# Kernel optimization log

Hardware: AMD Instinct MI355X
Metric: run time of the kernel (lower is better)

## Reference

```python
import jax, jax.numpy as jnp
import numpy as np

EPS = 1e-5

def _ln(x, g, b):
    mu = x.mean(-1, keepdims=True)
    var = ((x - mu) ** 2).mean(-1, keepdims=True)
    return (x - mu) / jnp.sqrt(var + EPS) * g + b


def setup_inputs() -> dict:
    key = jax.random.key(0)
    B, Hd, Wd = 4, 32, 32
    C, heads = 1024, 16
    N = Hd * Wd
    pd = (C // 4) // 4  # DynamicPosBias pos_dim = 64
    hid = 4 * C
    ks = jax.random.split(key, 24)

    def w(k, shape):
        return jax.random.normal(k, shape, jnp.float32) * 0.02

    inp = {
        'x': jax.random.normal(ks[0], (B, N, C), jnp.float32),
        'norm1_g': jnp.ones((C,), jnp.float32), 'norm1_b': jnp.zeros((C,), jnp.float32),
        'q_w': w(ks[1], (C, C)),              # no bias (qkv_bias=False)
        'kv_w': w(ks[2], (C, 2 * C)),
        'proj_w': w(ks[3], (C, C)), 'proj_b': jnp.zeros((C,), jnp.float32),
        'pos_proj_w': w(ks[4], (2, pd)), 'pos_proj_b': jnp.zeros((pd,), jnp.float32),
        'ln1_g': jnp.ones((pd,), jnp.float32), 'ln1_b': jnp.zeros((pd,), jnp.float32),
        'lin1_w': w(ks[5], (pd, pd)), 'lin1_b': jnp.zeros((pd,), jnp.float32),
        'ln2_g': jnp.ones((pd,), jnp.float32), 'ln2_b': jnp.zeros((pd,), jnp.float32),
        'lin2_w': w(ks[6], (pd, pd)), 'lin2_b': jnp.zeros((pd,), jnp.float32),
        'ln3_g': jnp.ones((pd,), jnp.float32), 'ln3_b': jnp.zeros((pd,), jnp.float32),
        'lin3_w': w(ks[7], (pd, heads)), 'lin3_b': jnp.zeros((heads,), jnp.float32),
        'norm2_g': jnp.ones((C,), jnp.float32), 'norm2_b': jnp.zeros((C,), jnp.float32),
        'fc1_w': w(ks[8], (C, hid)), 'fc1_b': jnp.zeros((hid,), jnp.float32),
        'fc2_w': w(ks[9], (hid, C)), 'fc2_b': jnp.zeros((C,), jnp.float32),
        'H': Hd, 'W': Wd,
    }
    return inp


def _rel_pos(H, W):
    # coordinate offsets fed to the bias MLP: [(2H-1)(2W-1), 2]
    ph = np.arange(1 - H, H)
    pw = np.arange(1 - W, W)
    bh, bw = np.meshgrid(ph, pw, indexing='ij')
    biases = np.stack([bh.ravel(), bw.ravel()], axis=1).astype(np.float32)
    # relative position index: [HW, HW]
    ch, cw = np.meshgrid(np.arange(H), np.arange(W), indexing='ij')
    flat = np.stack([ch.ravel(), cw.ravel()])                 # [2, HW]
    rel = flat[:, :, None] - flat[:, None, :]                 # [2, HW, HW]
    rel = rel.transpose(1, 2, 0)
    rel[:, :, 0] += H - 1
    rel[:, :, 1] += W - 1
    rel[:, :, 0] *= 2 * W - 1
    idx = rel.sum(-1)                                         # [HW, HW]
    return jnp.asarray(biases), jnp.asarray(idx)


def reference(x, norm1_g, norm1_b, q_w, kv_w, proj_w, proj_b,
              pos_proj_w, pos_proj_b, ln1_g, ln1_b, lin1_w, lin1_b,
              ln2_g, ln2_b, lin2_w, lin2_b, ln3_g, ln3_b, lin3_w, lin3_b,
              norm2_g, norm2_b, fc1_w, fc1_b, fc2_w, fc2_b, H, W):
    B, N, C = x.shape
    heads = lin3_w.shape[1]
    d = C // heads
    scale = d ** (-0.5)

    # --- HLGAttention (stage_index==4: group_size=(H,W), h0_token=None) ---
    xn = _ln(x, norm1_g, norm1_b)
    q = (xn @ q_w).reshape(B, N, heads, d).transpose(0, 2, 1, 3)   # [B,h,N,d]
    kv = (xn @ kv_w).reshape(B, N, 2, heads, d)
    k = kv[:, :, 0].transpose(0, 2, 1, 3)                          # [B,h,N,d]
    v = kv[:, :, 1].transpose(0, 2, 1, 3)
    attn = jnp.einsum('bhnd,bhmd->bhnm', q, k) * scale

    # dynamic relative position bias via small MLP + gather
    biases, rel_idx = _rel_pos(H, W)
    pos = biases @ pos_proj_w + pos_proj_b
    pos = jax.nn.relu(_ln(pos, ln1_g, ln1_b)) @ lin1_w + lin1_b
    pos = jax.nn.relu(_ln(pos, ln2_g, ln2_b)) @ lin2_w + lin2_b
    pos = jax.nn.relu(_ln(pos, ln3_g, ln3_b)) @ lin3_w + lin3_b    # [(2H-1)(2W-1), heads]
    rpb = pos[rel_idx]                                              # [N,N,heads]
    attn = attn + rpb.transpose(2, 0, 1)[None]

    attn = jax.nn.softmax(attn, axis=-1)
    out = jnp.einsum('bhnm,bhmd->bhnd', attn, v)
    out = out.transpose(0, 2, 1, 3).reshape(B, N, C)
    out = out @ proj_w + proj_b
    x = x + out

    # --- MLP block ---
    h = _ln(x, norm2_g, norm2_b) @ fc1_w + fc1_b
    h = jax.nn.gelu(h, approximate=False)
    x = x + (h @ fc2_w + fc2_b)
    return x
```

## Files before the change

### kernel.cpp

```cpp
#include <hip/hip_runtime.h>
#include <cstdint>
#include <cstddef>

typedef __attribute__((ext_vector_type(8))) __bf16 bf16x8;
typedef __attribute__((ext_vector_type(8))) unsigned short us8;
typedef __attribute__((ext_vector_type(4))) unsigned short us4;
typedef __attribute__((ext_vector_type(4))) float f32x4;
typedef __attribute__((ext_vector_type(16))) float f32x16;

#define DEVI static __device__ __forceinline__

DEVI unsigned short f2bf(float f) {
  union { float f; unsigned u; } v; v.f = f;
  unsigned r = v.u + 0x7fffu + ((v.u >> 16) & 1u);
  return (unsigned short)(r >> 16);
}

DEVI f32x4 mfma16(us8 a, us8 b, f32x4 c) {
  return __builtin_amdgcn_mfma_f32_16x16x32_bf16(
      __builtin_bit_cast(bf16x8, a), __builtin_bit_cast(bf16x8, b), c, 0, 0, 0);
}

DEVI f32x16 mfma32(us8 a, us8 b, f32x16 c) {
  return __builtin_amdgcn_mfma_f32_32x32x16_bf16(
      __builtin_bit_cast(bf16x8, a), __builtin_bit_cast(bf16x8, b), c, 0, 0, 0);
}

DEVI f32x4 fzero4() { f32x4 v = {0.f, 0.f, 0.f, 0.f}; return v; }

DEVI float gelu_f(float v) {
  float z = 0.7978845608f * v * (1.f + 0.044715f * v * v);
  float e = __expf(2.f * z);
  float r = 1.f / (e + 1.f);
  return v * (1.f - r);
}

DEVI unsigned pkbf(float lo, float hi) {
  unsigned r;
  asm("v_cvt_pk_bf16_f32 %0, %1, %2" : "=v"(r) : "v"(lo), "v"(hi));
  return r;
}

DEVI void pswap(unsigned& x, unsigned& y) {
  asm volatile("v_permlane32_swap_b32 %0, %1" : "+v"(x), "+v"(y));
}

DEVI void gload16(const unsigned short* g, unsigned short* l) {
  __builtin_amdgcn_global_load_lds(
      (const __attribute__((address_space(1))) unsigned int*)g,
      (__attribute__((address_space(3))) unsigned int*)l, 16, 0, 0);
}

DEVI void transpose_body(const float* __restrict__ w,
                         unsigned short* __restrict__ wt, int K, int N,
                         int kbi, int nbi, unsigned short (*tile)[65]) {
  const int t = threadIdx.x;
  const int kb = kbi * 64, nb = nbi * 64;
#pragma unroll
  for (int i = 0; i < 4; ++i) {
    int r = i * 16 + (t >> 4);
    int c = (t & 15) * 4;
    float4 v = *(const float4*)(w + (size_t)(kb + r) * N + nb + c);
    tile[r][c + 0] = f2bf(v.x);
    tile[r][c + 1] = f2bf(v.y);
    tile[r][c + 2] = f2bf(v.z);
    tile[r][c + 3] = f2bf(v.w);
  }
  __syncthreads();
#pragma unroll
  for (int i = 0; i < 4; ++i) {
    int n = i * 16 + (t >> 4);
    int k = (t & 15) * 4;
    us4 o;
    o[0] = tile[k + 0][n];
    o[1] = tile[k + 1][n];
    o[2] = tile[k + 2][n];
    o[3] = tile[k + 3][n];
    *(us4*)(wt + (size_t)(nb + n) * K + kb + k) = o;
  }
}

DEVI float pos_layer(float p, const float* __restrict__ g,
                     const float* __restrict__ be, const float* __restrict__ w,
                     const float* __restrict__ bb, int lane) {
  float s = p, sq = p * p;
#pragma unroll
  for (int m = 1; m < 64; m <<= 1) {
    s += __shfl_xor(s, m, 64);
    sq += __shfl_xor(sq, m, 64);
  }
  float mu = s * (1.f / 64.f);
  float var = sq * (1.f / 64.f) - mu * mu;
  float rstd = rsqrtf(var + 1e-5f);
  float y = fmaxf((p - mu) * rstd * g[lane] + be[lane], 0.f);
  float o = bb[lane];
  for (int k = 0; k < 64; ++k) {
    float yk = __shfl(y, k, 64);
    o += yk * w[k * 64 + lane];
  }
  return o;
}

__global__ __launch_bounds__(256)
void prep_kernel(const float* __restrict__ x, const float* __restrict__ n1g,
                 const float* __restrict__ n1b, unsigned short* __restrict__ xn,
                 const float* __restrict__ q_w, const float* __restrict__ kv_w,
                 const float* __restrict__ proj_w,
                 const float* __restrict__ fc1_w,
                 const float* __restrict__ fc2_w,
                 unsigned short* __restrict__ qkvT,
                 unsigned short* __restrict__ projT,
                 unsigned short* __restrict__ fc1T,
                 unsigned short* __restrict__ fc2T,
                 const float* __restrict__ pp_w, const float* __restrict__ pp_b,
                 const float* __restrict__ g1, const float* __restrict__ b1,
                 const float* __restrict__ w1, const float* __restrict__ bb1,
                 const float* __restrict__ g2, const float* __restrict__ b2,
                 const float* __restrict__ w2, const float* __restrict__ bb2,
                 const float* __restrict__ g3, const float* __restrict__ b3,
                 const float* __restrict__ w3, const float* __restrict__ bb3,
                 float* __restrict__ posT) {
  __shared__ unsigned short tile[64][65];
  __shared__ float ss[4], ssq[4];
  const int blk = blockIdx.x;
  const int tid = threadIdx.x;

  if (blk < 4096) {
    const int row = blk;
    const float* xr = x + (size_t)row * 1024;
    float4 v = *(const float4*)(xr + tid * 4);
    float s = v.x + v.y + v.z + v.w;
    float sq = v.x * v.x + v.y * v.y + v.z * v.z + v.w * v.w;
#pragma unroll
    for (int m = 1; m < 64; m <<= 1) {
      s += __shfl_xor(s, m, 64);
      sq += __shfl_xor(sq, m, 64);
    }
    const int wid = tid >> 6, lane = tid & 63;
    if (lane == 0) { ss[wid] = s; ssq[wid] = sq; }
    __syncthreads();
    s = ss[0] + ss[1] + ss[2] + ss[3];
    sq = ssq[0] + ssq[1] + ssq[2] + ssq[3];
    const float mu = s * (1.f / 1024.f);
    const float var = sq * (1.f / 1024.f) - mu * mu;
    const float rstd = rsqrtf(var + 1e-5f);
    const int c = tid * 4;
    float4 gv = *(const float4*)(n1g + c);
    float4 bv = *(const float4*)(n1b + c);
    us4 ov;
    ov[0] = f2bf((v.x - mu) * rstd * gv.x + bv.x);
    ov[1] = f2bf((v.y - mu) * rstd * gv.y + bv.y);
    ov[2] = f2bf((v.z - mu) * rstd * gv.z + bv.z);
    ov[3] = f2bf((v.w - mu) * rstd * gv.w + bv.w);
    *(us4*)(xn + (size_t)row * 1024 + c) = ov;
  } else if (blk < 5089) {
    const int wid = tid >> 6, lane = tid & 63;
    const int row = (blk - 4096) * 4 + wid;
    if (row >= 3969) return;
    const float bh = (float)(row / 63) - 31.f;
    const float bw = (float)(row % 63) - 31.f;
    float p = bh * pp_w[lane] + bw * pp_w[64 + lane] + pp_b[lane];
    p = pos_layer(p, g1, b1, w1, bb1, lane);
    p = pos_layer(p, g2, b2, w2, bb2, lane);
    float s = p, sq = p * p;
#pragma unroll
    for (int m = 1; m < 64; m <<= 1) {
      s += __shfl_xor(s, m, 64);
      sq += __shfl_xor(sq, m, 64);
    }
    float mu = s * (1.f / 64.f);
    float var = sq * (1.f / 64.f) - mu * mu;
    float rstd = rsqrtf(var + 1e-5f);
    float y = fmaxf((p - mu) * rstd * g3[lane] + b3[lane], 0.f);
    float o = 0.f;
    for (int k = 0; k < 64; ++k) {
      float yk = __shfl(y, k, 64);
      o += yk * w3[k * 16 + (lane & 15)];
    }
    if (lane < 16) posT[(size_t)lane * 3969 + row] = o + bb3[lane];
  } else if (blk < 5345) {
    const int lin = blk - 5089;
    transpose_body(q_w, qkvT, 1024, 1024, lin & 15, lin >> 4, tile);
  } else if (blk < 5857) {
    const int lin = blk - 5345;
    transpose_body(kv_w, qkvT + (size_t)1024 * 1024, 1024, 2048, lin & 15,
                   lin >> 4, tile);
  } else if (blk < 6113) {
    const int lin = blk - 5857;
    transpose_body(proj_w, projT, 1024, 1024, lin & 15, lin >> 4, tile);
  } else if (blk < 7137) {
    const int lin = blk - 6113;
    transpose_body(fc1_w, fc1T, 1024, 4096, lin & 15, lin >> 4, tile);
  } else {
    const int lin = blk - 7137;
    transpose_body(fc2_w, fc2T, 4096, 1024, lin & 63, lin >> 6, tile);
  }
}

__global__ __launch_bounds__(256)
void ln_kernel(const float* __restrict__ x, const float* __restrict__ g,
               const float* __restrict__ b, unsigned short* __restrict__ o) {
  const int row = blockIdx.x;
  const int tid = threadIdx.x;
  const float* xr = x + (size_t)row * 1024;
  float4 v = *(const float4*)(xr + tid * 4);
  float s = v.x + v.y + v.z + v.w;
  float sq = v.x * v.x + v.y * v.y + v.z * v.z + v.w * v.w;
#pragma unroll
  for (int m = 1; m < 64; m <<= 1) {
    s += __shfl_xor(s, m, 64);
    sq += __shfl_xor(sq, m, 64);
  }
  __shared__ float ss[4], ssq[4];
  const int wid = tid >> 6, lane = tid & 63;
  if (lane == 0) { ss[wid] = s; ssq[wid] = sq; }
  __syncthreads();
  s = ss[0] + ss[1] + ss[2] + ss[3];
  sq = ssq[0] + ssq[1] + ssq[2] + ssq[3];
  const float mu = s * (1.f / 1024.f);
  const float var = sq * (1.f / 1024.f) - mu * mu;
  const float rstd = rsqrtf(var + 1e-5f);
  const int c = tid * 4;
  float4 gv = *(const float4*)(g + c);
  float4 bv = *(const float4*)(b + c);
  us4 ov;
  ov[0] = f2bf((v.x - mu) * rstd * gv.x + bv.x);
  ov[1] = f2bf((v.y - mu) * rstd * gv.y + bv.y);
  ov[2] = f2bf((v.z - mu) * rstd * gv.z + bv.z);
  ov[3] = f2bf((v.w - mu) * rstd * gv.w + bv.w);
  *(us4*)(o + (size_t)row * 1024 + c) = ov;
}

template <int BM, int BN, bool HAS_BIAS, bool GELU_, bool HAS_RES,
          bool OUT_BF16, bool OUT_F32>
__global__ __launch_bounds__(256)
void gemm_bt(const unsigned short* __restrict__ A,
             const unsigned short* __restrict__ Bt,
             const float* __restrict__ bias, const float* __restrict__ res,
             unsigned short* __restrict__ outb, float* __restrict__ outf,
             int M, int N, int K) {
  constexpr int MT = BM / 32;
  constexpr int NT = BN / 32;
  __shared__ unsigned short As[BM * 128];
  __shared__ unsigned short Bs[BN * 128];
  const int tid = threadIdx.x;
  const int lane = tid & 63;
  const int wid = tid >> 6;
  const int lr = lane & 15, lg = lane >> 4;
  const int wr = wid >> 1, wc = wid & 1;
  const int brow = blockIdx.x, bcol = blockIdx.y;

  f32x4 acc[MT][NT];
#pragma unroll
  for (int mt = 0; mt < MT; ++mt)
#pragma unroll
    for (int nt = 0; nt < NT; ++nt) acc[mt][nt] = fzero4();

  const int sr = wid * 4 + (lane >> 4);
  const int sc = ((lane & 15) ^ ((sr & 7) << 1)) * 8;
  const unsigned short* Ag = A + (size_t)(brow * BM + sr) * K + sc;
  const unsigned short* Bg = Bt + (size_t)(bcol * BN + sr) * K + sc;

  const int nkb = K >> 7;
  for (int kb = 0; kb < nkb; ++kb) {
    __syncthreads();
#pragma unroll
    for (int q = 0; q < BM / 16; ++q)
      gload16(Ag + (size_t)(q * 16) * K + kb * 128,
              As + (q * 16 + wid * 4) * 128);
#pragma unroll
    for (int q = 0; q < BN / 16; ++q)
      gload16(Bg + (size_t)(q * 16) * K + kb * 128,
              Bs + (q * 16 + wid * 4) * 128);
    __syncthreads();
#pragma unroll
    for (int ks = 0; ks < 4; ++ks) {
      us8 af[MT], bfr[NT];
#pragma unroll
      for (int mt = 0; mt < MT; ++mt) {
        const int r = wr * (BM / 2) + mt * 16 + lr;
        const int ck = (ks * 4 + lg) ^ ((r & 7) << 1);
        af[mt] = *(const us8*)((const char*)As + r * 256 + ck * 16);
      }
#pragma unroll
      for (int nt = 0; nt < NT; ++nt) {
        const int r = wc * (BN / 2) + nt * 16 + lr;
        const int ck = (ks * 4 + lg) ^ ((r & 7) << 1);
        bfr[nt] = *(const us8*)((const char*)Bs + r * 256 + ck * 16);
      }
      __builtin_amdgcn_s_setprio(1);
#pragma unroll
      for (int mt = 0; mt < MT; ++mt)
#pragma unroll
        for (int nt = 0; nt < NT; ++nt)
          acc[mt][nt] = mfma16(af[mt], bfr[nt], acc[mt][nt]);
      __builtin_amdgcn_s_setprio(0);
    }
  }

#pragma unroll
  for (int mt = 0; mt < MT; ++mt) {
    const int row = brow * BM + wr * (BM / 2) + mt * 16 + 4 * lg;
#pragma unroll
    for (int nt = 0; nt < NT; ++nt) {
      const int col = bcol * BN + wc * (BN / 2) + nt * 16 + lr;
      float bsv = 0.f;
      if constexpr (HAS_BIAS) bsv = bias[col];
#pragma unroll
      for (int i = 0; i < 4; ++i) {
        float v = acc[mt][nt][i] + bsv;
        if constexpr (GELU_) v = gelu_f(v);
        if constexpr (HAS_RES) v += res[(size_t)(row + i) * N + col];
        if constexpr (OUT_F32) outf[(size_t)(row + i) * N + col] = v;
        if constexpr (OUT_BF16) outb[(size_t)(row + i) * N + col] = f2bf(v);
      }
    }
  }
}

__global__ __launch_bounds__(128)
void attn_kernel(const unsigned short* __restrict__ qkv,
                 const float* __restrict__ posT,
                 unsigned short* __restrict__ attnb) {
  __shared__ unsigned short Ks[64 * 64];
  __shared__ unsigned short Vt[64 * 64];

  const int tid = threadIdx.x;
  const int wid = tid >> 6;
  const int lane = tid & 63;
  const int ql = lane & 31;
  const int hi = lane >> 5;

  const int p = blockIdx.x;
  const int orig = (p & 7) * 128 + (p >> 3);
  const int b = orig >> 8;
  const int h = (orig >> 4) & 15;
  const int qt = orig & 15;

  const int LDQ = 3072;
  const int qg = qt * 64 + wid * 32 + ql;

  us8 qf[4];
  const unsigned short* qptr =
      qkv + (size_t)(b * 1024 + qg) * LDQ + h * 64 + 8 * hi;
#pragma unroll
  for (int db = 0; db < 4; ++db) qf[db] = *(const us8*)(qptr + db * 16);

  const float* pb = posT + (size_t)h * 3969;
  const int rb_q = ((qg >> 5) + 31) * 63 + (qg & 31) + 31 - 4 * hi;

  f32x16 oacc[2];
#pragma unroll
  for (int r = 0; r < 16; ++r) { oacc[0][r] = 0.f; oacc[1][r] = 0.f; }
  float mreg = -1e30f, lsum = 0.f;

  const int ksr = tid >> 1;
  const int ksc = (tid & 1) * 32;
  const int vd0 = (tid & 15) * 4;
  const int vk0 = (tid >> 4) * 8;

  const unsigned short* kbase = qkv + (size_t)(b * 1024) * LDQ + 1024 + h * 64;
  const unsigned short* vbase = qkv + (size_t)(b * 1024) * LDQ + 2048 + h * 64;

  us8 pk[4];
  us4 pvv[8];
#pragma unroll
  for (int j = 0; j < 4; ++j)
    pk[j] = *(const us8*)(kbase + (size_t)ksr * LDQ + ksc + j * 8);
#pragma unroll
  for (int j = 0; j < 8; ++j)
    pvv[j] = *(const us4*)(vbase + (size_t)(vk0 + j) * LDQ + vd0);

  for (int kt = 0; kt < 16; ++kt) {
    __syncthreads();
    {
      char* ksb = (char*)Ks;
      const int swr = (ksr & 7) << 4;
#pragma unroll
      for (int j = 0; j < 4; ++j)
        *(us8*)(ksb + ksr * 128 + (((ksc + j * 8) * 2) ^ swr)) = pk[j];
      char* vtb = (char*)Vt;
      const int cbase = vk0 << 1;
#pragma unroll
      for (int u = 0; u < 4; ++u) {
        const int d = vd0 + u;
        const int addr = d * 128 + (cbase ^ ((d & 7) << 4));
        us4 lo, hi4;
        lo[0] = pvv[0][u]; lo[1] = pvv[1][u]; lo[2] = pvv[2][u]; lo[3] = pvv[3][u];
        hi4[0] = pvv[4][u]; hi4[1] = pvv[5][u]; hi4[2] = pvv[6][u]; hi4[3] = pvv[7][u];
        *(us4*)(vtb + addr) = lo;
        *(us4*)(vtb + addr + 8) = hi4;
      }
    }
    __syncthreads();

    if (kt < 15) {
      const unsigned short* kb2 = kbase + (size_t)((kt + 1) * 64) * LDQ;
      const unsigned short* vb2 = vbase + (size_t)((kt + 1) * 64) * LDQ;
#pragma unroll
      for (int j = 0; j < 4; ++j)
        pk[j] = *(const us8*)(kb2 + (size_t)ksr * LDQ + ksc + j * 8);
#pragma unroll
      for (int j = 0; j < 8; ++j)
        pvv[j] = *(const us4*)(vb2 + (size_t)(vk0 + j) * LDQ + vd0);
    }

    f32x16 st0, st1;
#pragma unroll
    for (int r = 0; r < 16; ++r) { st0[r] = 0.f; st1[r] = 0.f; }
    const char* ksb = (const char*)Ks;
    const int kswz = (ql & 7) << 4;
    __builtin_amdgcn_s_setprio(1);
#pragma unroll
    for (int db = 0; db < 4; ++db) {
      const int coff = (db * 32 + 16 * hi) ^ kswz;
      us8 kf0 = *(const us8*)(ksb + ql * 128 + coff);
      us8 kf1 = *(const us8*)(ksb + (32 + ql) * 128 + coff);
      st0 = mfma32(kf0, qf[db], st0);
      st1 = mfma32(kf1, qf[db], st1);
    }
    __builtin_amdgcn_s_setprio(0);

    float sv0[16], sv1[16];
    const float* pb0 = pb + (rb_q - 63 * (2 * kt));
    const float* pb1 = pb0 - 63;
    float mm[16];
#pragma unroll
    for (int r = 0; r < 16; ++r) {
      const int roff = (r & 3) + 8 * (r >> 2);
      float a = st0[r] * 0.125f + pb0[-roff];
      float c = st1[r] * 0.125f + pb1[-roff];
      sv0[r] = a;
      sv1[r] = c;
      mm[r] = fmaxf(a, c);
    }
#pragma unroll
    for (int w = 8; w >= 1; w >>= 1)
#pragma unroll
      for (int r = 0; r < w; ++r) mm[r] = fmaxf(mm[r], mm[r + w]);
    float pm = fmaxf(mm[0], __shfl_xor(mm[0], 32, 64));

    if (pm > mreg + 8.f) {
      const float f = __expf(mreg - pm);
      lsum *= f;
#pragma unroll
      for (int r = 0; r < 16; ++r) { oacc[0][r] *= f; oacc[1][r] *= f; }
      mreg = pm;
    }

    float ts[16];
#pragma unroll
    for (int r = 0; r < 16; ++r) {
      float e0 = __expf(sv0[r] - mreg);
      float e1 = __expf(sv1[r] - mreg);
      sv0[r] = e0;
      sv1[r] = e1;
      ts[r] = e0 + e1;
    }
#pragma unroll
    for (int w = 8; w >= 1; w >>= 1)
#pragma unroll
      for (int r = 0; r < w; ++r) ts[r] += ts[r + w];
    lsum += ts[0];

    const char* vtb = (const char*)Vt;
    auto pvfrag = [&](const float* sv, int kb) {
      const int B0 = (kb & 1) * 8;
      unsigned a0 = pkbf(sv[B0 + 0], sv[B0 + 1]);
      unsigned a1 = pkbf(sv[B0 + 2], sv[B0 + 3]);
      unsigned b0 = pkbf(sv[B0 + 4], sv[B0 + 5]);
      unsigned b1 = pkbf(sv[B0 + 6], sv[B0 + 7]);
      pswap(a0, b0);
      pswap(a1, b1);
      union { us8 s; unsigned u[4]; } fu;
      fu.u[0] = a0; fu.u[1] = a1; fu.u[2] = b0; fu.u[3] = b1;
      const int coff = (kb * 32 + 16 * hi) ^ kswz;
      us8 vf0 = *(const us8*)(vtb + ql * 128 + coff);
      us8 vf1 = *(const us8*)(vtb + (32 + ql) * 128 + coff);
      __builtin_amdgcn_s_setprio(1);
      oacc[0] = mfma32(vf0, fu.s, oacc[0]);
      oacc[1] = mfma32(vf1, fu.s, oacc[1]);
      __builtin_amdgcn_s_setprio(0);
    };
    pvfrag(sv0, 0);
    pvfrag(sv0, 1);
    pvfrag(sv1, 2);
    pvfrag(sv1, 3);
  }

  lsum += __shfl_xor(lsum, 32, 64);
  const float inv = 1.f / lsum;
  unsigned short* orow = attnb + (size_t)(b * 1024 + qg) * 1024 + h * 64;
#pragma unroll
  for (int dm = 0; dm < 2; ++dm)
#pragma unroll
    for (int r = 0; r < 16; ++r) {
      const int d = dm * 32 + (r & 3) + 8 * (r >> 2) + 4 * hi;
      orow[d] = f2bf(oacc[dm][r] * inv);
    }
}

extern "C" void kernel_launch(void* const* d_in, const int* in_sizes, int n_in,
                              void* d_out, int out_size, void* d_ws,
                              size_t ws_size, hipStream_t stream) {
  const float* x = (const float*)d_in[0];
  const float* n1g = (const float*)d_in[1];
  const float* n1b = (const float*)d_in[2];
  const float* q_w = (const float*)d_in[3];
  const float* kv_w = (const float*)d_in[4];
  const float* proj_w = (const float*)d_in[5];
  const float* proj_b = (const float*)d_in[6];
  const float* pp_w = (const float*)d_in[7];
  const float* pp_b = (const float*)d_in[8];
  const float* ln1g = (const float*)d_in[9];
  const float* ln1b = (const float*)d_in[10];
  const float* lin1w = (const float*)d_in[11];
  const float* lin1b = (const float*)d_in[12];
  const float* ln2g = (const float*)d_in[13];
  const float* ln2b = (const float*)d_in[14];
  const float* lin2w = (const float*)d_in[15];
  const float* lin2b = (const float*)d_in[16];
  const float* ln3g = (const float*)d_in[17];
  const float* ln3b = (const float*)d_in[18];
  const float* lin3w = (const float*)d_in[19];
  const float* lin3b = (const float*)d_in[20];
  const float* n2g = (const float*)d_in[21];
  const float* n2b = (const float*)d_in[22];
  const float* fc1_w = (const float*)d_in[23];
  const float* fc1_b = (const float*)d_in[24];
  const float* fc2_w = (const float*)d_in[25];
  const float* fc2_b = (const float*)d_in[26];
  float* out = (float*)d_out;

  char* ws = (char*)d_ws;
  const size_t MB = 1024ull * 1024ull;
  unsigned short* qkvT = (unsigned short*)(ws + 0 * MB);
  unsigned short* projT = (unsigned short*)(ws + 6 * MB);
  unsigned short* fc1T = (unsigned short*)(ws + 8 * MB);
  unsigned short* fc2T = (unsigned short*)(ws + 16 * MB);
  unsigned short* xn = (unsigned short*)(ws + 24 * MB);
  unsigned short* qkv = (unsigned short*)(ws + 32 * MB);
  unsigned short* attnb = (unsigned short*)(ws + 56 * MB);
  float* x1 = (float*)(ws + 64 * MB);
  unsigned short* x2n = (unsigned short*)(ws + 80 * MB);
  unsigned short* hb = (unsigned short*)(ws + 88 * MB);
  float* posT = (float*)(ws + 120 * MB);

  prep_kernel<<<8161, 256, 0, stream>>>(
      x, n1g, n1b, xn, q_w, kv_w, proj_w, fc1_w, fc2_w, qkvT, projT, fc1T,
      fc2T, pp_w, pp_b, ln1g, ln1b, lin1w, lin1b, ln2g, ln2b, lin2w, lin2b,
      ln3g, ln3b, lin3w, lin3b, posT);

  gemm_bt<128, 128, false, false, false, true, false>
      <<<dim3(32, 24), 256, 0, stream>>>(xn, qkvT, nullptr, nullptr, qkv,
                                         nullptr, 4096, 3072, 1024);

  attn_kernel<<<1024, 128, 0, stream>>>(qkv, posT, attnb);

  gemm_bt<64, 128, true, false, true, false, true>
      <<<dim3(64, 8), 256, 0, stream>>>(attnb, projT, proj_b, x, nullptr, x1,
                                        4096, 1024, 1024);

  ln_kernel<<<4096, 256, 0, stream>>>(x1, n2g, n2b, x2n);

  gemm_bt<128, 128, true, true, false, true, false>
      <<<dim3(32, 32), 256, 0, stream>>>(x2n, fc1T, fc1_b, nullptr, hb,
                                         nullptr, 4096, 4096, 1024);

  gemm_bt<64, 128, true, false, true, false, true>
      <<<dim3(64, 8), 256, 0, stream>>>(hb, fc2T, fc2_b, x1, nullptr, out,
                                        4096, 1024, 4096);

  (void)in_sizes; (void)n_in; (void)out_size; (void)ws_size;
}
```

Before: 223.4 us.

## Double-buffer GEMM LDS tiles with async prefetch two K-blocks ahead

```diff
diff --git a/kernel.cpp b/kernel.cpp
--- a/kernel.cpp
+++ b/kernel.cpp
@@ -49,6 +49,21 @@
   __builtin_amdgcn_global_load_lds(
       (const __attribute__((address_space(1))) unsigned int*)g,
       (__attribute__((address_space(3))) unsigned int*)l, 16, 0, 0);
+}
+
+template <int N>
+DEVI void wait_vm() {
+  if constexpr (N == 0) asm volatile("s_waitcnt vmcnt(0)" ::: "memory");
+  else if constexpr (N == 6) asm volatile("s_waitcnt vmcnt(6)" ::: "memory");
+  else if constexpr (N == 8) asm volatile("s_waitcnt vmcnt(8)" ::: "memory");
+  else if constexpr (N == 12) asm volatile("s_waitcnt vmcnt(12)" ::: "memory");
+  else if constexpr (N == 16) asm volatile("s_waitcnt vmcnt(16)" ::: "memory");
+  __builtin_amdgcn_sched_barrier(0);
+}
+
+DEVI void wait_lgkm0() {
+  asm volatile("s_waitcnt lgkmcnt(0)" ::: "memory");
+  __builtin_amdgcn_sched_barrier(0);
 }
 
 DEVI void transpose_body(const float* __restrict__ w,
@@ -241,8 +256,9 @@
              int M, int N, int K) {
   constexpr int MT = BM / 32;
   constexpr int NT = BN / 32;
-  __shared__ unsigned short As[BM * 128];
-  __shared__ unsigned short Bs[BN * 128];
+  constexpr int S = BM / 32 + BN / 32;
+  __shared__ unsigned short As[2][BM * 64];
+  __shared__ unsigned short Bs[2][BN * 64];
   const int tid = threadIdx.x;
   const int lane = tid & 63;
   const int wid = tid >> 6;
@@ -256,37 +272,45 @@
 #pragma unroll
     for (int nt = 0; nt < NT; ++nt) acc[mt][nt] = fzero4();
 
-  const int sr = wid * 4 + (lane >> 4);
-  const int sc = ((lane & 15) ^ ((sr & 7) << 1)) * 8;
+  const int sr = wid * 8 + (lane >> 3);
+  const int sc = ((lane & 7) ^ (sr & 7)) * 8;
   const unsigned short* Ag = A + (size_t)(brow * BM + sr) * K + sc;
   const unsigned short* Bg = Bt + (size_t)(bcol * BN + sr) * K + sc;
 
-  const int nkb = K >> 7;
+  auto stage = [&](int buf, int kb) {
+#pragma unroll
+    for (int q = 0; q < BM / 32; ++q)
+      gload16(Ag + (size_t)(q * 32) * K + kb * 64,
+              &As[buf][(q * 32 + wid * 8) * 64]);
+#pragma unroll
+    for (int q = 0; q < BN / 32; ++q)
+      gload16(Bg + (size_t)(q * 32) * K + kb * 64,
+              &Bs[buf][(q * 32 + wid * 8) * 64]);
+  };
+
+  const int nkb = K >> 6;
+  stage(0, 0);
+  stage(1, 1);
+  wait_vm<S>();
+  __builtin_amdgcn_s_barrier();
+  __builtin_amdgcn_sched_barrier(0);
+
+  int cur = 0;
   for (int kb = 0; kb < nkb; ++kb) {
-    __syncthreads();
-#pragma unroll
-    for (int q = 0; q < BM / 16; ++q)
-      gload16(Ag + (size_t)(q * 16) * K + kb * 128,
-              As + (q * 16 + wid * 4) * 128);
-#pragma unroll
-    for (int q = 0; q < BN / 16; ++q)
-      gload16(Bg + (size_t)(q * 16) * K + kb * 128,
-              Bs + (q * 16 + wid * 4) * 128);
-    __syncthreads();
-#pragma unroll
-    for (int ks = 0; ks < 4; ++ks) {
+#pragma unroll
+    for (int ks = 0; ks < 2; ++ks) {
       us8 af[MT], bfr[NT];
 #pragma unroll
       for (int mt = 0; mt < MT; ++mt) {
         const int r = wr * (BM / 2) + mt * 16 + lr;
-        const int ck = (ks * 4 + lg) ^ ((r & 7) << 1);
-        af[mt] = *(const us8*)((const char*)As + r * 256 + ck * 16);
+        const int ck = (ks * 4 + lg) ^ (r & 7);
+        af[mt] = *(const us8*)((const char*)&As[cur][0] + r * 128 + ck * 16);
       }
 #pragma unroll
       for (int nt = 0; nt < NT; ++nt) {
         const int r = wc * (BN / 2) + nt * 16 + lr;
-        const int ck = (ks * 4 + lg) ^ ((r & 7) << 1);
-        bfr[nt] = *(const us8*)((const char*)Bs + r * 256 + ck * 16);
+        const int ck = (ks * 4 + lg) ^ (r & 7);
+        bfr[nt] = *(const us8*)((const char*)&Bs[cur][0] + r * 128 + ck * 16);
       }
       __builtin_amdgcn_s_setprio(1);
 #pragma unroll
@@ -296,6 +320,18 @@
           acc[mt][nt] = mfma16(af[mt], bfr[nt], acc[mt][nt]);
       __builtin_amdgcn_s_setprio(0);
     }
+    wait_lgkm0();
+    __builtin_amdgcn_s_barrier();
+    __builtin_amdgcn_sched_barrier(0);
+    if (kb + 2 < nkb) {
+      stage(cur, kb + 2);
+      wait_vm<S>();
+    } else {
+      wait_vm<0>();
+    }
+    __builtin_amdgcn_s_barrier();
+    __builtin_amdgcn_sched_barrier(0);
+    cur ^= 1;
   }
 
 #pragma unroll
```

After: 248.7 us. 1.11x slower.
